# Kernel tuning notes

Hardware: AMD Instinct MI355X
Metric: run time of the kernel (lower is better)

Reference implementation:

```python
import jax, jax.numpy as jnp
import numpy as np

B, T, E, H = 1, 4096, 1024, 16
HD = E // H  # 64
SCALE = 8.0 / HD  # scaling='d' per Tensor Programs V


def setup_inputs() -> dict:
    key = jax.random.key(0)
    ks = jax.random.split(key, 7)
    s = 1.0 / np.sqrt(E)
    return {
        "q": jax.random.normal(ks[0], (B, T, E), jnp.float32),
        "k": jax.random.normal(ks[1], (B, T, E), jnp.float32),
        "v": jax.random.normal(ks[2], (B, T, E), jnp.float32),
        "Wq": jax.random.normal(ks[3], (E, E), jnp.float32) * s,
        "Wk": jax.random.normal(ks[4], (E, E), jnp.float32) * s,
        "Wv": jax.random.normal(ks[5], (E, E), jnp.float32) * s,
        "Wo": jax.random.normal(ks[6], (E, E), jnp.float32) * s,
    }


def reference(q, k, v, Wq, Wk, Wv, Wo):
    # bias-free linear projections (nn.Linear: y = x @ W.T)
    qp = q @ Wq.T
    kp = k @ Wk.T
    vp = v @ Wv.T
    # b t (h d) -> b h t d
    qh = qp.reshape(B, T, H, HD).transpose(0, 2, 1, 3)
    kh = kp.reshape(B, T, H, HD).transpose(0, 2, 1, 3)
    vh = vp.reshape(B, T, H, HD).transpose(0, 2, 1, 3)
    scores = jnp.einsum('bhqd,bhkd->bhqk', qh, kh) * SCALE
    # causal mask: positions k > q masked with -inf
    causal = jnp.tril(jnp.ones((T, T), dtype=bool))
    scores = jnp.where(causal[None, None], scores, -jnp.inf)
    probs = jax.nn.softmax(scores, axis=-1)
    out = jnp.einsum('bhqk,bhkd->bhqd', probs, vh)
    # b h t d -> b t (h d)
    out = out.transpose(0, 2, 1, 3).reshape(B, T, E)
    return out @ Wo.T
```

## Files before the change

kernel.cpp:

```cpp
#include <hip/hip_runtime.h>
#include <hip/hip_bf16.h>

#define T_DIM 4096
#define E_DIM 1024
#define H_DIM 16
#define HD_DIM 64
#define LOG2E_F 1.4426950408889634f
#define QSCALE_F (0.125f * LOG2E_F)

typedef __bf16 bf16_t;
typedef __bf16 bf16x8 __attribute__((ext_vector_type(8)));
typedef __bf16 bf16x4 __attribute__((ext_vector_type(4)));
typedef float  f32x4  __attribute__((ext_vector_type(4)));

__device__ inline void stage8(bf16_t* dst, const float* src) {
  const f32x4* s4 = (const f32x4*)src;
  f32x4 a = s4[0], b = s4[1];
  bf16x8 o;
  o[0] = (bf16_t)a[0]; o[1] = (bf16_t)a[1]; o[2] = (bf16_t)a[2]; o[3] = (bf16_t)a[3];
  o[4] = (bf16_t)b[0]; o[5] = (bf16_t)b[1]; o[6] = (bf16_t)b[2]; o[7] = (bf16_t)b[3];
  *(bf16x8*)dst = o;
}
__device__ inline void stage8(bf16_t* dst, const bf16_t* src) {
  *(bf16x8*)dst = *(const bf16x8*)src;
}

__device__ inline void gld_lds16(const bf16_t* g, bf16_t* l) {
  __builtin_amdgcn_global_load_lds(
      (const __attribute__((address_space(1))) unsigned int*)g,
      (__attribute__((address_space(3))) unsigned int*)l, 16, 0, 0);
}

__device__ inline float fexp2(float x) {
  float r;
  asm("v_exp_f32 %0, %1" : "=v"(r) : "v"(x));
  return r;
}

__device__ inline void block_sync() {
  asm volatile("" ::: "memory");
  __builtin_amdgcn_s_barrier();
  asm volatile("" ::: "memory");
}

__global__ __launch_bounds__(256) void cvt_all(
    const float* __restrict__ q, const float* __restrict__ k, const float* __restrict__ v,
    const float* __restrict__ Wq, const float* __restrict__ Wk,
    const float* __restrict__ Wv, const float* __restrict__ Wo,
    bf16_t* qb, bf16_t* kb, bf16_t* vb,
    bf16_t* Wqb, bf16_t* Wkb, bf16_t* Wvb, bf16_t* Wob) {
  for (int u = blockIdx.x * 256 + threadIdx.x; u < 2097152; u += gridDim.x * 256) {
    const float* s; bf16_t* d; int i;
    if (u < 1572864) {
      int seg = u >> 19, off = u & 524287;
      s = seg == 0 ? q : (seg == 1 ? k : v);
      d = seg == 0 ? qb : (seg == 1 ? kb : vb);
      i = off;
    } else {
      int w = u - 1572864;
      int seg = w >> 17, off = w & 131071;
      s = seg == 0 ? Wq : seg == 1 ? Wk : seg == 2 ? Wv : Wo;
      d = seg == 0 ? Wqb : seg == 1 ? Wkb : seg == 2 ? Wvb : Wob;
      i = off;
    }
    stage8(d + (size_t)i * 8, s + (size_t)i * 8);
  }
}

template <int MF, int NF, typename TC>
__device__ __forceinline__ void gemm_body(const bf16_t* __restrict__ A,
                                          const bf16_t* __restrict__ B,
                                          TC* __restrict__ C,
                                          int ldC, int bm, int bn, float cs) {
  constexpr int BM = 32 * MF, BN = 32 * NF;
  __shared__ alignas(16) bf16_t As[BM][64];
  __shared__ alignas(16) bf16_t Bs[BN][64];
  const int tid  = threadIdx.x;
  const int lane = tid & 63, w = tid >> 6;
  const int g = lane >> 4, l15 = lane & 15;
  const int wr = w >> 1, wc = w & 1;

  f32x4 acc[MF][NF] = {};

  for (int kt = 0; kt < 1024; kt += 64) {
    if (kt) __syncthreads();
#pragma unroll
    for (int p = 0; p < MF; ++p) {
      int s = p * 256 + tid;
      int row = s >> 3, c = s & 7;
      int cg = c ^ (row & 7);
      gld_lds16(&A[(size_t)(bm + row) * 1024 + kt + cg * 8], &As[0][0] + s * 8);
    }
#pragma unroll
    for (int p = 0; p < NF; ++p) {
      int s = p * 256 + tid;
      int row = s >> 3, c = s & 7;
      int cg = c ^ (row & 7);
      gld_lds16(&B[(size_t)(bn + row) * 1024 + kt + cg * 8], &Bs[0][0] + s * 8);
    }
    asm volatile("s_waitcnt vmcnt(0)" ::: "memory");
    __syncthreads();

#pragma unroll
    for (int hh = 0; hh < 2; ++hh) {
      bf16x8 af[MF], bfr[NF];
#pragma unroll
      for (int m = 0; m < MF; ++m) {
        int row = wr * (16 * MF) + m * 16 + l15;
        af[m] = *(const bf16x8*)(&As[0][0] + row * 64 + (((hh * 4 + g) ^ (row & 7)) * 8));
      }
#pragma unroll
      for (int n = 0; n < NF; ++n) {
        int row = wc * (16 * NF) + n * 16 + l15;
        bfr[n] = *(const bf16x8*)(&Bs[0][0] + row * 64 + (((hh * 4 + g) ^ (row & 7)) * 8));
      }
#pragma unroll
      for (int m = 0; m < MF; ++m)
#pragma unroll
        for (int n = 0; n < NF; ++n)
          acc[m][n] = __builtin_amdgcn_mfma_f32_16x16x32_bf16(af[m], bfr[n], acc[m][n], 0, 0, 0);
    }
  }

#pragma unroll
  for (int m = 0; m < MF; ++m)
#pragma unroll
    for (int n = 0; n < NF; ++n)
#pragma unroll
      for (int r = 0; r < 4; ++r) {
        int row = bm + wr * (16 * MF) + m * 16 + g * 4 + r;
        int col = bn + wc * (16 * NF) + n * 16 + l15;
        C[(size_t)row * ldC + col] = (TC)(acc[m][n][r] * cs);
      }
}

__global__ __launch_bounds__(256) void proj_qkv(
    const bf16_t* __restrict__ qb, const bf16_t* __restrict__ kb,
    const bf16_t* __restrict__ vb,
    const bf16_t* __restrict__ Wqb, const bf16_t* __restrict__ Wkb,
    const bf16_t* __restrict__ Wvb,
    bf16_t* Qp, bf16_t* Kp, bf16_t* Vt) {
  const int bid = blockIdx.x;
  const int which = bid >> 8, t = bid & 255;
  const bf16_t *A, *B; bf16_t* C; int ldC, bm, bn; float cs;
  if (which == 0) {
    A = qb;  B = Wqb; C = Qp; ldC = 1024;
    bm = (t >> 3) * 128; bn = (t & 7) * 128; cs = QSCALE_F;
  } else if (which == 1) {
    A = kb;  B = Wkb; C = Kp; ldC = 1024;
    bm = (t >> 3) * 128; bn = (t & 7) * 128; cs = 1.0f;
  } else {
    A = Wvb; B = vb;  C = Vt; ldC = 4096;
    bm = (t >> 5) * 128; bn = (t & 31) * 128; cs = 1.0f;
  }
  gemm_body<4, 4, bf16_t>(A, B, C, ldC, bm, bn, cs);
}

__global__ __launch_bounds__(256) void gemm_fin(const bf16_t* __restrict__ A,
                                                const bf16_t* __restrict__ B,
                                                float* __restrict__ C) {
  gemm_body<2, 4, float>(A, B, C, 1024, blockIdx.y * 64, blockIdx.x * 128, 1.0f);
}

template <typename TA, typename TB, typename TC>
__global__ __launch_bounds__(256) void gemm_bt(const TA* __restrict__ A,
                                               const TB* __restrict__ B,
                                               TC* __restrict__ C,
                                               int M, int N, int K, float cscale) {
  __shared__ alignas(16) bf16_t As[128][40];
  __shared__ alignas(16) bf16_t Bs[128][40];
  const int tid  = threadIdx.x;
  const int lane = tid & 63, w = tid >> 6;
  const int g = lane >> 4, l15 = lane & 15;
  const int wr = w >> 1, wc = w & 1;
  const int bm = blockIdx.y * 128, bn = blockIdx.x * 128;

  f32x4 acc[4][4] = {};

  for (int kt = 0; kt < K; kt += 32) {
    __syncthreads();
#pragma unroll
    for (int i = 0; i < 2; ++i) {
      int vv  = tid + i * 256;
      int row = vv >> 2, c8 = (vv & 3) * 8;
      stage8(&As[row][c8], &A[(size_t)(bm + row) * K + kt + c8]);
      stage8(&Bs[row][c8], &B[(size_t)(bn + row) * K + kt + c8]);
    }
    __syncthreads();

    bf16x8 af[4], bfr[4];
#pragma unroll
    for (int m = 0; m < 4; ++m)
      af[m] = *(const bf16x8*)&As[wr * 64 + m * 16 + l15][g * 8];
#pragma unroll
    for (int n = 0; n < 4; ++n)
      bfr[n] = *(const bf16x8*)&Bs[wc * 64 + n * 16 + l15][g * 8];
#pragma unroll
    for (int m = 0; m < 4; ++m)
#pragma unroll
      for (int n = 0; n < 4; ++n)
        acc[m][n] = __builtin_amdgcn_mfma_f32_16x16x32_bf16(af[m], bfr[n], acc[m][n], 0, 0, 0);
  }

#pragma unroll
  for (int m = 0; m < 4; ++m)
#pragma unroll
    for (int n = 0; n < 4; ++n)
#pragma unroll
      for (int r = 0; r < 4; ++r) {
        int row = bm + wr * 64 + m * 16 + g * 4 + r;
        int col = bn + wc * 64 + n * 16 + l15;
        C[(size_t)row * N + col] = (TC)(acc[m][n][r] * cscale);
      }
}

__global__ __launch_bounds__(256) void attn_fwd(const bf16_t* __restrict__ Qp,
                                                const bf16_t* __restrict__ Kp,
                                                const bf16_t* __restrict__ Vt,
                                                bf16_t* __restrict__ Oattn) {
  const int bid = blockIdx.x;
  const int h  = bid & 15;
  const int qi = 63 - (bid >> 4);
  const int tid = threadIdx.x, lane = tid & 63, w = tid >> 6;
  const int g = lane >> 4, l15 = lane & 15;
  const int qrow = qi * 64 + w * 16;

  __shared__ alignas(16) bf16_t Ks[2][64][64];
  __shared__ alignas(16) bf16_t Vs[3][64][64];
  __shared__ alignas(16) bf16_t Plds[4][16][72];

  bf16x8 qf[2];
  {
    const bf16_t* qp = &Qp[(size_t)(qrow + l15) * E_DIM + h * 64 + g * 8];
    qf[0] = *(const bf16x8*)qp;
    qf[1] = *(const bf16x8*)(qp + 32);
  }

  const int row0 = tid >> 3, c0 = tid & 7;
  const int cgo = (c0 ^ (row0 & 7)) * 8;
  const bf16_t* srcK0 = Kp + (size_t)row0 * E_DIM + h * 64 + cgo;
  const bf16_t* srcK1 = srcK0 + (size_t)32 * E_DIM;
  const bf16_t* srcV0 = Vt + (size_t)(h * 64 + row0) * T_DIM + cgo;
  const bf16_t* srcV1 = srcV0 + (size_t)32 * T_DIM;
  bf16_t* KsAll = &Ks[0][0][0];
  bf16_t* VsAll = &Vs[0][0][0];
  const size_t KADV = (size_t)64 * E_DIM;
  const int nt = qi + 1;

  auto issue = [&](int t) {
    bf16_t* kd = KsAll + (t & 1) * 4096;
    bf16_t* vd = VsAll + (t % 3) * 4096;
    gld_lds16(srcK0 + (size_t)t * KADV, kd + tid * 8);
    gld_lds16(srcK1 + (size_t)t * KADV, kd + (256 + tid) * 8);
    gld_lds16(srcV0 + (size_t)t * 64,   vd + tid * 8);
    gld_lds16(srcV1 + (size_t)t * 64,   vd + (256 + tid) * 8);
  };

  f32x4 acc[4] = {};
  float m_s = -1e30f, l_s = 0.f;

  auto pv = [&](int t) {
    const char* Vb = (const char*)(VsAll + (t % 3) * 4096);
    bf16x8 pf0 = *(const bf16x8*)&Plds[w][l15][g * 8];
    bf16x8 pf1 = *(const bf16x8*)&Plds[w][l15][32 + g * 8];
#pragma unroll
    for (int c = 0; c < 4; ++c) {
      const int vr = c * 16 + l15;
      const char* rp = Vb + vr * 128;
      const int sw = (vr & 7) << 4;
      bf16x8 v0 = *(const bf16x8*)(rp + ((g * 16) ^ sw));
      bf16x8 v1 = *(const bf16x8*)(rp + ((64 + g * 16) ^ sw));
      acc[c] = __builtin_amdgcn_mfma_f32_16x16x32_bf16(v0, pf0, acc[c], 0, 0, 0);
      acc[c] = __builtin_amdgcn_mfma_f32_16x16x32_bf16(v1, pf1, acc[c], 0, 0, 0);
    }
  };

  issue(0);

  for (int j = 0; j < nt; ++j) {
    asm volatile("s_waitcnt vmcnt(0)" ::: "memory");
    block_sync();
    if (j + 1 < nt) issue(j + 1);

    __builtin_amdgcn_s_setprio(1);
    if (j > 0) pv(j - 1);

    const char* Kb = (const char*)(KsAll + (j & 1) * 4096);
    f32x4 s[4] = {};
#pragma unroll
    for (int j16 = 0; j16 < 4; ++j16) {
      const int r0 = j16 * 16 + l15;
      const char* rp = Kb + r0 * 128;
      const int sw = (r0 & 7) << 4;
      bf16x8 k0 = *(const bf16x8*)(rp + ((g * 16) ^ sw));
      bf16x8 k1 = *(const bf16x8*)(rp + ((64 + g * 16) ^ sw));
      s[j16] = __builtin_amdgcn_mfma_f32_16x16x32_bf16(k0, qf[0], s[j16], 0, 0, 0);
      s[j16] = __builtin_amdgcn_mfma_f32_16x16x32_bf16(k1, qf[1], s[j16], 0, 0, 0);
    }
    __builtin_amdgcn_s_setprio(0);

    if (j == nt - 1) {
      const int kb = j * 64;
#pragma unroll
      for (int j16 = 0; j16 < 4; ++j16)
#pragma unroll
        for (int r = 0; r < 4; ++r)
          if (kb + j16 * 16 + g * 4 + r > qrow + l15) s[j16][r] = -1e30f;
    }

    float pmax = s[0][0];
#pragma unroll
    for (int j16 = 0; j16 < 4; ++j16)
#pragma unroll
      for (int r = 0; r < 4; ++r) pmax = fmaxf(pmax, s[j16][r]);
    pmax = fmaxf(pmax, __shfl_xor(pmax, 16));
    pmax = fmaxf(pmax, __shfl_xor(pmax, 32));

    if (!__all(pmax <= m_s + 11.0f)) {
      float mn = fmaxf(m_s, pmax);
      float sc = fexp2(m_s - mn);
      m_s = mn;
      l_s *= sc;
#pragma unroll
      for (int c = 0; c < 4; ++c)
#pragma unroll
        for (int r = 0; r < 4; ++r) acc[c][r] *= sc;
    }

    float ps = 0.f;
#pragma unroll
    for (int j16 = 0; j16 < 4; ++j16)
#pragma unroll
      for (int r = 0; r < 4; ++r) {
        s[j16][r] = fexp2(s[j16][r] - m_s);
        ps += s[j16][r];
      }
    ps += __shfl_xor(ps, 16);
    ps += __shfl_xor(ps, 32);
    l_s += ps;

#pragma unroll
    for (int j16 = 0; j16 < 4; ++j16) {
      bf16x4 pk;
      pk[0] = (bf16_t)s[j16][0]; pk[1] = (bf16_t)s[j16][1];
      pk[2] = (bf16_t)s[j16][2]; pk[3] = (bf16_t)s[j16][3];
      *(bf16x4*)&Plds[w][l15][j16 * 16 + g * 4] = pk;
    }
  }

  pv(nt - 1);

  const float inv = 1.0f / l_s;
#pragma unroll
  for (int c = 0; c < 4; ++c) {
    bf16x4 o;
#pragma unroll
    for (int r = 0; r < 4; ++r) o[r] = (bf16_t)(acc[c][r] * inv);
    *(bf16x4*)&Oattn[(size_t)(qrow + l15) * E_DIM + h * 64 + c * 16 + g * 4] = o;
  }
}

extern "C" void kernel_launch(void* const* d_in, const int* in_sizes, int n_in,
                              void* d_out, int out_size, void* d_ws, size_t ws_size,
                              hipStream_t stream) {
  const float* q  = (const float*)d_in[0];
  const float* k  = (const float*)d_in[1];
  const float* v  = (const float*)d_in[2];
  const float* Wq = (const float*)d_in[3];
  const float* Wk = (const float*)d_in[4];
  const float* Wv = (const float*)d_in[5];
  const float* Wo = (const float*)d_in[6];
  float* out = (float*)d_out;

  const size_t TE = (size_t)T_DIM * E_DIM;
  const size_t EE = (size_t)E_DIM * E_DIM;
  dim3 blk(256);

  if (ws_size >= (size_t)56 * 1024 * 1024) {
    bf16_t* qb  = (bf16_t*)d_ws;
    bf16_t* kb  = qb + TE;
    bf16_t* vb  = kb + TE;
    bf16_t* Wqb = vb + TE;
    bf16_t* Wkb = Wqb + EE;
    bf16_t* Wvb = Wkb + EE;
    bf16_t* Wob = Wvb + EE;
    bf16_t* Qp  = Wob + EE;
    bf16_t* Kp  = Qp + TE;
    bf16_t* Vt  = Kp + TE;
    bf16_t* Oa  = qb;

    cvt_all<<<2048, blk, 0, stream>>>(q, k, v, Wq, Wk, Wv, Wo,
                                      qb, kb, vb, Wqb, Wkb, Wvb, Wob);
    proj_qkv<<<dim3(768), blk, 0, stream>>>(qb, kb, vb, Wqb, Wkb, Wvb, Qp, Kp, Vt);
    attn_fwd<<<dim3(1024), blk, 0, stream>>>(Qp, Kp, Vt, Oa);
    gemm_fin<<<dim3(8, 64), blk, 0, stream>>>(Oa, Wob, out);
  } else {
    bf16_t* Qp = (bf16_t*)d_ws;
    bf16_t* Kp = Qp + TE;
    bf16_t* Vt = Kp + TE;
    bf16_t* Oa = Vt + TE;
    gemm_bt<float, float, bf16_t><<<dim3(8, 32), blk, 0, stream>>>(q, Wq, Qp, T_DIM, E_DIM, E_DIM, QSCALE_F);
    gemm_bt<float, float, bf16_t><<<dim3(8, 32), blk, 0, stream>>>(k, Wk, Kp, T_DIM, E_DIM, E_DIM, 1.0f);
    gemm_bt<float, float, bf16_t><<<dim3(32, 8), blk, 0, stream>>>(Wv, v, Vt, E_DIM, T_DIM, E_DIM, 1.0f);
    attn_fwd<<<dim3(1024), blk, 0, stream>>>(Qp, Kp, Vt, Oa);
    gemm_bt<bf16_t, float, float><<<dim3(8, 32), blk, 0, stream>>>(Oa, Wo, out, T_DIM, E_DIM, E_DIM, 1.0f);
  }
}
```

Before: 141.0 us.

## Halve attention KV tile to 32 keys and defer row-sum reduction

The attention kernel now steps through keys in 32-wide tiles instead of 64, so each iteration loads one K and one V chunk per thread, and the LDS buffers and the P buffer shrink with a new XOR swizzle. The per-lane partial row sum is kept local and reduced across lanes only once at the end, and the row-max shuffles run only when a rescale is needed. Masking is applied to every tile that overlaps the diagonal rather than only the last one. This lowers LDS use per block and per-iteration shuffle work, at the cost of twice as many iterations, each with a barrier and a wait on memory.

```diff
diff --git a/kernel.cpp b/kernel.cpp
--- a/kernel.cpp
+++ b/kernel.cpp
@@ -225,9 +225,9 @@
   const int g = lane >> 4, l15 = lane & 15;
   const int qrow = qi * 64 + w * 16;
 
-  __shared__ alignas(16) bf16_t Ks[2][64][64];
-  __shared__ alignas(16) bf16_t Vs[3][64][64];
-  __shared__ alignas(16) bf16_t Plds[4][16][72];
+  __shared__ alignas(16) bf16_t Ks[2][32][64];
+  __shared__ alignas(16) bf16_t Vs[3][64][32];
+  __shared__ alignas(16) bf16_t Plds[4][16][32];
 
   bf16x8 qf[2];
   {
@@ -236,42 +236,34 @@
     qf[1] = *(const bf16x8*)(qp + 32);
   }
 
-  const int row0 = tid >> 3, c0 = tid & 7;
-  const int cgo = (c0 ^ (row0 & 7)) * 8;
-  const bf16_t* srcK0 = Kp + (size_t)row0 * E_DIM + h * 64 + cgo;
-  const bf16_t* srcK1 = srcK0 + (size_t)32 * E_DIM;
-  const bf16_t* srcV0 = Vt + (size_t)(h * 64 + row0) * T_DIM + cgo;
-  const bf16_t* srcV1 = srcV0 + (size_t)32 * T_DIM;
+  const int krow = tid >> 3;
+  const int kcg  = ((tid & 7) ^ (krow & 7)) * 8;
+  const bf16_t* srcK = Kp + (size_t)krow * E_DIM + h * 64 + kcg;
+  const int vrow = tid >> 2;
+  const int vcg  = ((tid & 3) ^ (vrow & 3)) * 8;
+  const bf16_t* srcV = Vt + (size_t)(h * 64 + vrow) * T_DIM + vcg;
   bf16_t* KsAll = &Ks[0][0][0];
   bf16_t* VsAll = &Vs[0][0][0];
-  const size_t KADV = (size_t)64 * E_DIM;
-  const int nt = qi + 1;
+  const size_t KADV = (size_t)32 * E_DIM;
+  const int nt = 2 * qi + 2;
 
   auto issue = [&](int t) {
-    bf16_t* kd = KsAll + (t & 1) * 4096;
-    bf16_t* vd = VsAll + (t % 3) * 4096;
-    gld_lds16(srcK0 + (size_t)t * KADV, kd + tid * 8);
-    gld_lds16(srcK1 + (size_t)t * KADV, kd + (256 + tid) * 8);
-    gld_lds16(srcV0 + (size_t)t * 64,   vd + tid * 8);
-    gld_lds16(srcV1 + (size_t)t * 64,   vd + (256 + tid) * 8);
+    gld_lds16(srcK + (size_t)t * KADV, KsAll + (t & 1) * 2048 + tid * 8);
+    gld_lds16(srcV + (size_t)t * 32,   VsAll + (t % 3) * 2048 + tid * 8);
   };
 
   f32x4 acc[4] = {};
-  float m_s = -1e30f, l_s = 0.f;
-
+  float m_s = -1e30f, l_p = 0.f;
+
+  const int psw = (g ^ (l15 & 3)) << 4;
   auto pv = [&](int t) {
-    const char* Vb = (const char*)(VsAll + (t % 3) * 4096);
-    bf16x8 pf0 = *(const bf16x8*)&Plds[w][l15][g * 8];
-    bf16x8 pf1 = *(const bf16x8*)&Plds[w][l15][32 + g * 8];
+    const char* Vb = (const char*)(VsAll + (t % 3) * 2048);
+    bf16x8 pf0 = *(const bf16x8*)((const char*)&Plds[w][l15][0] + psw);
 #pragma unroll
     for (int c = 0; c < 4; ++c) {
       const int vr = c * 16 + l15;
-      const char* rp = Vb + vr * 128;
-      const int sw = (vr & 7) << 4;
-      bf16x8 v0 = *(const bf16x8*)(rp + ((g * 16) ^ sw));
-      bf16x8 v1 = *(const bf16x8*)(rp + ((64 + g * 16) ^ sw));
+      bf16x8 v0 = *(const bf16x8*)(Vb + vr * 64 + psw);
       acc[c] = __builtin_amdgcn_mfma_f32_16x16x32_bf16(v0, pf0, acc[c], 0, 0, 0);
-      acc[c] = __builtin_amdgcn_mfma_f32_16x16x32_bf16(v1, pf1, acc[c], 0, 0, 0);
     }
   };
 
@@ -285,10 +277,10 @@
     __builtin_amdgcn_s_setprio(1);
     if (j > 0) pv(j - 1);
 
-    const char* Kb = (const char*)(KsAll + (j & 1) * 4096);
-    f32x4 s[4] = {};
-#pragma unroll
-    for (int j16 = 0; j16 < 4; ++j16) {
+    const char* Kb = (const char*)(KsAll + (j & 1) * 2048);
+    f32x4 s[2] = {};
+#pragma unroll
+    for (int j16 = 0; j16 < 2; ++j16) {
       const int r0 = j16 * 16 + l15;
       const char* rp = Kb + r0 * 128;
       const int sw = (r0 & 7) << 4;
@@ -299,28 +291,24 @@
     }
     __builtin_amdgcn_s_setprio(0);
 
-    if (j == nt - 1) {
-      const int kb = j * 64;
-#pragma unroll
-      for (int j16 = 0; j16 < 4; ++j16)
+    const int kb = j * 32;
+    if (kb + 31 > qrow) {
+#pragma unroll
+      for (int j16 = 0; j16 < 2; ++j16)
 #pragma unroll
         for (int r = 0; r < 4; ++r)
           if (kb + j16 * 16 + g * 4 + r > qrow + l15) s[j16][r] = -1e30f;
     }
 
-    float pmax = s[0][0];
-#pragma unroll
-    for (int j16 = 0; j16 < 4; ++j16)
-#pragma unroll
-      for (int r = 0; r < 4; ++r) pmax = fmaxf(pmax, s[j16][r]);
-    pmax = fmaxf(pmax, __shfl_xor(pmax, 16));
-    pmax = fmaxf(pmax, __shfl_xor(pmax, 32));
-
+    float pmax = fmaxf(fmaxf(fmaxf(s[0][0], s[0][1]), fmaxf(s[0][2], s[0][3])),
+                       fmaxf(fmaxf(s[1][0], s[1][1]), fmaxf(s[1][2], s[1][3])));
     if (!__all(pmax <= m_s + 11.0f)) {
-      float mn = fmaxf(m_s, pmax);
+      float rm = fmaxf(pmax, __shfl_xor(pmax, 16));
+      rm = fmaxf(rm, __shfl_xor(rm, 32));
+      float mn = fmaxf(m_s, rm);
       float sc = fexp2(m_s - mn);
       m_s = mn;
-      l_s *= sc;
+      l_p *= sc;
 #pragma unroll
       for (int c = 0; c < 4; ++c)
 #pragma unroll
@@ -329,28 +317,29 @@
 
     float ps = 0.f;
 #pragma unroll
-    for (int j16 = 0; j16 < 4; ++j16)
+    for (int j16 = 0; j16 < 2; ++j16)
 #pragma unroll
       for (int r = 0; r < 4; ++r) {
         s[j16][r] = fexp2(s[j16][r] - m_s);
         ps += s[j16][r];
       }
-    ps += __shfl_xor(ps, 16);
-    ps += __shfl_xor(ps, 32);
-    l_s += ps;
-
-#pragma unroll
-    for (int j16 = 0; j16 < 4; ++j16) {
+    l_p += ps;
+
+#pragma unroll
+    for (int j16 = 0; j16 < 2; ++j16) {
       bf16x4 pk;
       pk[0] = (bf16_t)s[j16][0]; pk[1] = (bf16_t)s[j16][1];
       pk[2] = (bf16_t)s[j16][2]; pk[3] = (bf16_t)s[j16][3];
-      *(bf16x4*)&Plds[w][l15][j16 * 16 + g * 4] = pk;
+      *(bf16x4*)&Plds[w][l15][(((2 * j16 + (g >> 1)) ^ (l15 & 3)) * 8) + (g & 1) * 4] = pk;
     }
   }
 
   pv(nt - 1);
 
-  const float inv = 1.0f / l_s;
+  float lt = l_p;
+  lt += __shfl_xor(lt, 16);
+  lt += __shfl_xor(lt, 32);
+  const float inv = 1.0f / lt;
 #pragma unroll
   for (int c = 0; c < 4; ++c) {
     bf16x4 o;
```

New measurement: 151.4 us. +7.4%, slower.

## Pair causal query tiles per block for balanced attention work

Applied to the files above, without the earlier changes.

Each attention block now handles two query tiles, one at 63-ii and one at ii, so every block does the same total number of key tiles (65). The grid is halved to 512 blocks. This removes the load imbalance and tail effect of causal attention, at the cost of fewer blocks and a serial second pass with an extra barrier. The row max cross-lane shuffle now runs only inside the rescale branch. The row-sum reduction is moved out of the loop to the end of each pass.

```diff
diff --git a/kernel.cpp b/kernel.cpp
--- a/kernel.cpp
+++ b/kernel.cpp
@@ -220,21 +220,13 @@
                                                 bf16_t* __restrict__ Oattn) {
   const int bid = blockIdx.x;
   const int h  = bid & 15;
-  const int qi = 63 - (bid >> 4);
+  const int ii = bid >> 4;
   const int tid = threadIdx.x, lane = tid & 63, w = tid >> 6;
   const int g = lane >> 4, l15 = lane & 15;
-  const int qrow = qi * 64 + w * 16;
 
   __shared__ alignas(16) bf16_t Ks[2][64][64];
   __shared__ alignas(16) bf16_t Vs[3][64][64];
   __shared__ alignas(16) bf16_t Plds[4][16][72];
-
-  bf16x8 qf[2];
-  {
-    const bf16_t* qp = &Qp[(size_t)(qrow + l15) * E_DIM + h * 64 + g * 8];
-    qf[0] = *(const bf16x8*)qp;
-    qf[1] = *(const bf16x8*)(qp + 32);
-  }
 
   const int row0 = tid >> 3, c0 = tid & 7;
   const int cgo = (c0 ^ (row0 & 7)) * 8;
@@ -245,7 +237,6 @@
   bf16_t* KsAll = &Ks[0][0][0];
   bf16_t* VsAll = &Vs[0][0][0];
   const size_t KADV = (size_t)64 * E_DIM;
-  const int nt = qi + 1;
 
   auto issue = [&](int t) {
     bf16_t* kd = KsAll + (t & 1) * 4096;
@@ -256,8 +247,8 @@
     gld_lds16(srcV1 + (size_t)t * 64,   vd + (256 + tid) * 8);
   };
 
-  f32x4 acc[4] = {};
-  float m_s = -1e30f, l_s = 0.f;
+  f32x4 acc[4];
+  float m_s, l_p;
 
   auto pv = [&](int t) {
     const char* Vb = (const char*)(VsAll + (t % 3) * 4096);
@@ -275,88 +266,108 @@
     }
   };
 
-  issue(0);
-
-  for (int j = 0; j < nt; ++j) {
-    asm volatile("s_waitcnt vmcnt(0)" ::: "memory");
-    block_sync();
-    if (j + 1 < nt) issue(j + 1);
-
-    __builtin_amdgcn_s_setprio(1);
-    if (j > 0) pv(j - 1);
-
-    const char* Kb = (const char*)(KsAll + (j & 1) * 4096);
-    f32x4 s[4] = {};
-#pragma unroll
-    for (int j16 = 0; j16 < 4; ++j16) {
-      const int r0 = j16 * 16 + l15;
-      const char* rp = Kb + r0 * 128;
-      const int sw = (r0 & 7) << 4;
-      bf16x8 k0 = *(const bf16x8*)(rp + ((g * 16) ^ sw));
-      bf16x8 k1 = *(const bf16x8*)(rp + ((64 + g * 16) ^ sw));
-      s[j16] = __builtin_amdgcn_mfma_f32_16x16x32_bf16(k0, qf[0], s[j16], 0, 0, 0);
-      s[j16] = __builtin_amdgcn_mfma_f32_16x16x32_bf16(k1, qf[1], s[j16], 0, 0, 0);
-    }
-    __builtin_amdgcn_s_setprio(0);
-
-    if (j == nt - 1) {
-      const int kb = j * 64;
+  for (int pass = 0; pass < 2; ++pass) {
+    const int qi = pass ? ii : 63 - ii;
+    const int qrow = qi * 64 + w * 16;
+    const int nt = qi + 1;
+
+    bf16x8 qf[2];
+    {
+      const bf16_t* qp = &Qp[(size_t)(qrow + l15) * E_DIM + h * 64 + g * 8];
+      qf[0] = *(const bf16x8*)qp;
+      qf[1] = *(const bf16x8*)(qp + 32);
+    }
+#pragma unroll
+    for (int c = 0; c < 4; ++c)
+#pragma unroll
+      for (int r = 0; r < 4; ++r) acc[c][r] = 0.f;
+    m_s = -1e30f; l_p = 0.f;
+
+    if (pass) block_sync();
+    issue(0);
+
+    for (int j = 0; j < nt; ++j) {
+      asm volatile("s_waitcnt vmcnt(0)" ::: "memory");
+      block_sync();
+      if (j + 1 < nt) issue(j + 1);
+
+      __builtin_amdgcn_s_setprio(1);
+      if (j > 0) pv(j - 1);
+
+      const char* Kb = (const char*)(KsAll + (j & 1) * 4096);
+      f32x4 s[4] = {};
+#pragma unroll
+      for (int j16 = 0; j16 < 4; ++j16) {
+        const int r0 = j16 * 16 + l15;
+        const char* rp = Kb + r0 * 128;
+        const int sw = (r0 & 7) << 4;
+        bf16x8 k0 = *(const bf16x8*)(rp + ((g * 16) ^ sw));
+        bf16x8 k1 = *(const bf16x8*)(rp + ((64 + g * 16) ^ sw));
+        s[j16] = __builtin_amdgcn_mfma_f32_16x16x32_bf16(k0, qf[0], s[j16], 0, 0, 0);
+        s[j16] = __builtin_amdgcn_mfma_f32_16x16x32_bf16(k1, qf[1], s[j16], 0, 0, 0);
+      }
+      __builtin_amdgcn_s_setprio(0);
+
+      if (j == nt - 1) {
+        const int kb = j * 64;
+#pragma unroll
+        for (int j16 = 0; j16 < 4; ++j16)
+#pragma unroll
+          for (int r = 0; r < 4; ++r)
+            if (kb + j16 * 16 + g * 4 + r > qrow + l15) s[j16][r] = -1e30f;
+      }
+
+      float pmax = s[0][0];
 #pragma unroll
       for (int j16 = 0; j16 < 4; ++j16)
 #pragma unroll
-        for (int r = 0; r < 4; ++r)
-          if (kb + j16 * 16 + g * 4 + r > qrow + l15) s[j16][r] = -1e30f;
-    }
-
-    float pmax = s[0][0];
-#pragma unroll
-    for (int j16 = 0; j16 < 4; ++j16)
-#pragma unroll
-      for (int r = 0; r < 4; ++r) pmax = fmaxf(pmax, s[j16][r]);
-    pmax = fmaxf(pmax, __shfl_xor(pmax, 16));
-    pmax = fmaxf(pmax, __shfl_xor(pmax, 32));
-
-    if (!__all(pmax <= m_s + 11.0f)) {
-      float mn = fmaxf(m_s, pmax);
-      float sc = fexp2(m_s - mn);
-      m_s = mn;
-      l_s *= sc;
-#pragma unroll
-      for (int c = 0; c < 4; ++c)
-#pragma unroll
-        for (int r = 0; r < 4; ++r) acc[c][r] *= sc;
-    }
-
-    float ps = 0.f;
-#pragma unroll
-    for (int j16 = 0; j16 < 4; ++j16)
-#pragma unroll
-      for (int r = 0; r < 4; ++r) {
-        s[j16][r] = fexp2(s[j16][r] - m_s);
-        ps += s[j16][r];
-      }
-    ps += __shfl_xor(ps, 16);
-    ps += __shfl_xor(ps, 32);
-    l_s += ps;
-
-#pragma unroll
-    for (int j16 = 0; j16 < 4; ++j16) {
-      bf16x4 pk;
-      pk[0] = (bf16_t)s[j16][0]; pk[1] = (bf16_t)s[j16][1];
-      pk[2] = (bf16_t)s[j16][2]; pk[3] = (bf16_t)s[j16][3];
-      *(bf16x4*)&Plds[w][l15][j16 * 16 + g * 4] = pk;
-    }
-  }
-
-  pv(nt - 1);
-
-  const float inv = 1.0f / l_s;
-#pragma unroll
-  for (int c = 0; c < 4; ++c) {
-    bf16x4 o;
-#pragma unroll
-    for (int r = 0; r < 4; ++r) o[r] = (bf16_t)(acc[c][r] * inv);
-    *(bf16x4*)&Oattn[(size_t)(qrow + l15) * E_DIM + h * 64 + c * 16 + g * 4] = o;
+        for (int r = 0; r < 4; ++r) pmax = fmaxf(pmax, s[j16][r]);
+
+      if (!__all(pmax <= m_s + 11.0f)) {
+        float rm = fmaxf(pmax, __shfl_xor(pmax, 16));
+        rm = fmaxf(rm, __shfl_xor(rm, 32));
+        float mn = fmaxf(m_s, rm);
+        float sc = fexp2(m_s - mn);
+        m_s = mn;
+        l_p *= sc;
+#pragma unroll
+        for (int c = 0; c < 4; ++c)
+#pragma unroll
+          for (int r = 0; r < 4; ++r) acc[c][r] *= sc;
+      }
+
+      float ps = 0.f;
+#pragma unroll
+      for (int j16 = 0; j16 < 4; ++j16)
+#pragma unroll
+        for (int r = 0; r < 4; ++r) {
+          s[j16][r] = fexp2(s[j16][r] - m_s);
+          ps += s[j16][r];
+        }
+      l_p += ps;
+
+#pragma unroll
+      for (int j16 = 0; j16 < 4; ++j16) {
+        bf16x4 pk;
+        pk[0] = (bf16_t)s[j16][0]; pk[1] = (bf16_t)s[j16][1];
+        pk[2] = (bf16_t)s[j16][2]; pk[3] = (bf16_t)s[j16][3];
+        *(bf16x4*)&Plds[w][l15][j16 * 16 + g * 4] = pk;
+      }
+    }
+
+    pv(nt - 1);
+
+    float lt = l_p;
+    lt += __shfl_xor(lt, 16);
+    lt += __shfl_xor(lt, 32);
+    const float inv = 1.0f / lt;
+#pragma unroll
+    for (int c = 0; c < 4; ++c) {
+      bf16x4 o;
+#pragma unroll
+      for (int r = 0; r < 4; ++r) o[r] = (bf16_t)(acc[c][r] * inv);
+      *(bf16x4*)&Oattn[(size_t)(qrow + l15) * E_DIM + h * 64 + c * 16 + g * 4] = o;
+    }
   }
 }
 
@@ -392,7 +403,7 @@
     cvt_all<<<2048, blk, 0, stream>>>(q, k, v, Wq, Wk, Wv, Wo,
                                       qb, kb, vb, Wqb, Wkb, Wvb, Wob);
     proj_qkv<<<dim3(768), blk, 0, stream>>>(qb, kb, vb, Wqb, Wkb, Wvb, Qp, Kp, Vt);
-    attn_fwd<<<dim3(1024), blk, 0, stream>>>(Qp, Kp, Vt, Oa);
+    attn_fwd<<<dim3(512), blk, 0, stream>>>(Qp, Kp, Vt, Oa);
     gemm_fin<<<dim3(8, 64), blk, 0, stream>>>(Oa, Wob, out);
   } else {
     bf16_t* Qp = (bf16_t*)d_ws;
@@ -402,7 +413,7 @@
     gemm_bt<float, float, bf16_t><<<dim3(8, 32), blk, 0, stream>>>(q, Wq, Qp, T_DIM, E_DIM, E_DIM, QSCALE_F);
     gemm_bt<float, float, bf16_t><<<dim3(8, 32), blk, 0, stream>>>(k, Wk, Kp, T_DIM, E_DIM, E_DIM, 1.0f);
     gemm_bt<float, float, bf16_t><<<dim3(32, 8), blk, 0, stream>>>(Wv, v, Vt, E_DIM, T_DIM, E_DIM, 1.0f);
-    attn_fwd<<<dim3(1024), blk, 0, stream>>>(Qp, Kp, Vt, Oa);
+    attn_fwd<<<dim3(512), blk, 0, stream>>>(Qp, Kp, Vt, Oa);
     gemm_bt<bf16_t, float, float><<<dim3(8, 32), blk, 0, stream>>>(Oa, Wo, out, T_DIM, E_DIM, E_DIM, 1.0f);
   }
 }
```

Result: faster. 131.6 us (-6.7%).

## Use 32x32 MFMA attention tiles with 128-row query blocks and MFMA row sums

Applied to the files above, without the earlier changes.

Rewrites the attention kernel so each block handles 128 query rows, with 32 rows per wave, and uses 32x32x16 MFMAs in place of 16x16x32. This halves the grid and doubles K/V tile reuse per block load. The softmax row sum now comes from an extra MFMA against a ones vector instead of shuffle reductions. The causal schedule is remapped to pair heavy and light query blocks, and the P LDS layout is swizzled. In exchange it uses more accumulator registers and adds an extra MFMA per PV step, and the larger blocks may reduce occupancy and load balance.

```diff
diff --git a/kernel.cpp b/kernel.cpp
--- a/kernel.cpp
+++ b/kernel.cpp
@@ -12,6 +12,7 @@
 typedef __bf16 bf16x8 __attribute__((ext_vector_type(8)));
 typedef __bf16 bf16x4 __attribute__((ext_vector_type(4)));
 typedef float  f32x4  __attribute__((ext_vector_type(4)));
+typedef float  f32x16 __attribute__((ext_vector_type(16)));
 
 __device__ inline void stage8(bf16_t* dst, const float* src) {
   const f32x4* s4 = (const f32x4*)src;
@@ -219,22 +220,27 @@
                                                 const bf16_t* __restrict__ Vt,
                                                 bf16_t* __restrict__ Oattn) {
   const int bid = blockIdx.x;
-  const int h  = bid & 15;
-  const int qi = 63 - (bid >> 4);
+  const int h   = bid & 15;
+  const int idx = bid >> 4;
+  const int qi  = idx < 16 ? 31 - idx : idx - 16;
   const int tid = threadIdx.x, lane = tid & 63, w = tid >> 6;
-  const int g = lane >> 4, l15 = lane & 15;
-  const int qrow = qi * 64 + w * 16;
+  const int ql = lane & 31, hl = lane >> 5;
+  const int qrow = qi * 128 + w * 32;
 
   __shared__ alignas(16) bf16_t Ks[2][64][64];
   __shared__ alignas(16) bf16_t Vs[3][64][64];
-  __shared__ alignas(16) bf16_t Plds[4][16][72];
-
-  bf16x8 qf[2];
+  __shared__ alignas(16) bf16_t Plds[4][32][64];
+
+  bf16x8 qf[4];
   {
-    const bf16_t* qp = &Qp[(size_t)(qrow + l15) * E_DIM + h * 64 + g * 8];
-    qf[0] = *(const bf16x8*)qp;
-    qf[1] = *(const bf16x8*)(qp + 32);
-  }
+    const bf16_t* qp = &Qp[(size_t)(qrow + ql) * E_DIM + h * 64 + 8 * hl];
+#pragma unroll
+    for (int ds = 0; ds < 4; ++ds) qf[ds] = *(const bf16x8*)(qp + ds * 16);
+  }
+
+  bf16x8 ones;
+#pragma unroll
+  for (int i = 0; i < 8; ++i) ones[i] = (bf16_t)1.0f;
 
   const int row0 = tid >> 3, c0 = tid & 7;
   const int cgo = (c0 ^ (row0 & 7)) * 8;
@@ -245,7 +251,7 @@
   bf16_t* KsAll = &Ks[0][0][0];
   bf16_t* VsAll = &Vs[0][0][0];
   const size_t KADV = (size_t)64 * E_DIM;
-  const int nt = qi + 1;
+  const int nt = 2 * qi + 2;
 
   auto issue = [&](int t) {
     bf16_t* kd = KsAll + (t & 1) * 4096;
@@ -256,22 +262,26 @@
     gld_lds16(srcV1 + (size_t)t * 64,   vd + (256 + tid) * 8);
   };
 
-  f32x4 acc[4] = {};
-  float m_s = -1e30f, l_s = 0.f;
+  f32x16 acc0 = {}, acc1 = {};
+  f32x16 acc_l = {};
+  float m_s = -1e30f;
+
+  const char* Pw = (const char*)&Plds[w][0][0];
+  const int x7 = ql & 7;
 
   auto pv = [&](int t) {
     const char* Vb = (const char*)(VsAll + (t % 3) * 4096);
-    bf16x8 pf0 = *(const bf16x8*)&Plds[w][l15][g * 8];
-    bf16x8 pf1 = *(const bf16x8*)&Plds[w][l15][32 + g * 8];
-#pragma unroll
-    for (int c = 0; c < 4; ++c) {
-      const int vr = c * 16 + l15;
-      const char* rp = Vb + vr * 128;
-      const int sw = (vr & 7) << 4;
-      bf16x8 v0 = *(const bf16x8*)(rp + ((g * 16) ^ sw));
-      bf16x8 v1 = *(const bf16x8*)(rp + ((64 + g * 16) ^ sw));
-      acc[c] = __builtin_amdgcn_mfma_f32_16x16x32_bf16(v0, pf0, acc[c], 0, 0, 0);
-      acc[c] = __builtin_amdgcn_mfma_f32_16x16x32_bf16(v1, pf1, acc[c], 0, 0, 0);
+    bf16x8 pf[4];
+#pragma unroll
+    for (int ks = 0; ks < 4; ++ks)
+      pf[ks] = *(const bf16x8*)(Pw + ql * 128 + (((2 * ks + hl) ^ x7) << 4));
+#pragma unroll
+    for (int ks = 0; ks < 4; ++ks) {
+      bf16x8 v0 = *(const bf16x8*)(Vb + ql * 128        + (((2 * ks + hl) ^ x7) << 4));
+      bf16x8 v1 = *(const bf16x8*)(Vb + (32 + ql) * 128 + (((2 * ks + hl) ^ x7) << 4));
+      acc0 = __builtin_amdgcn_mfma_f32_32x32x16_bf16(v0, pf[ks], acc0, 0, 0, 0);
+      acc1 = __builtin_amdgcn_mfma_f32_32x32x16_bf16(v1, pf[ks], acc1, 0, 0, 0);
+      acc_l = __builtin_amdgcn_mfma_f32_32x32x16_bf16(ones, pf[ks], acc_l, 0, 0, 0);
     }
   };
 
@@ -286,77 +296,84 @@
     if (j > 0) pv(j - 1);
 
     const char* Kb = (const char*)(KsAll + (j & 1) * 4096);
-    f32x4 s[4] = {};
-#pragma unroll
-    for (int j16 = 0; j16 < 4; ++j16) {
-      const int r0 = j16 * 16 + l15;
-      const char* rp = Kb + r0 * 128;
-      const int sw = (r0 & 7) << 4;
-      bf16x8 k0 = *(const bf16x8*)(rp + ((g * 16) ^ sw));
-      bf16x8 k1 = *(const bf16x8*)(rp + ((64 + g * 16) ^ sw));
-      s[j16] = __builtin_amdgcn_mfma_f32_16x16x32_bf16(k0, qf[0], s[j16], 0, 0, 0);
-      s[j16] = __builtin_amdgcn_mfma_f32_16x16x32_bf16(k1, qf[1], s[j16], 0, 0, 0);
+    f32x16 s0 = {}, s1 = {};
+#pragma unroll
+    for (int ds = 0; ds < 4; ++ds) {
+      bf16x8 k0 = *(const bf16x8*)(Kb + ql * 128        + (((2 * ds + hl) ^ x7) << 4));
+      bf16x8 k1 = *(const bf16x8*)(Kb + (32 + ql) * 128 + (((2 * ds + hl) ^ x7) << 4));
+      s0 = __builtin_amdgcn_mfma_f32_32x32x16_bf16(k0, qf[ds], s0, 0, 0, 0);
+      s1 = __builtin_amdgcn_mfma_f32_32x32x16_bf16(k1, qf[ds], s1, 0, 0, 0);
     }
     __builtin_amdgcn_s_setprio(0);
 
-    if (j == nt - 1) {
-      const int kb = j * 64;
-#pragma unroll
-      for (int j16 = 0; j16 < 4; ++j16)
-#pragma unroll
-        for (int r = 0; r < 4; ++r)
-          if (kb + j16 * 16 + g * 4 + r > qrow + l15) s[j16][r] = -1e30f;
-    }
-
-    float pmax = s[0][0];
-#pragma unroll
-    for (int j16 = 0; j16 < 4; ++j16)
-#pragma unroll
-      for (int r = 0; r < 4; ++r) pmax = fmaxf(pmax, s[j16][r]);
-    pmax = fmaxf(pmax, __shfl_xor(pmax, 16));
-    pmax = fmaxf(pmax, __shfl_xor(pmax, 32));
+    const int kb = j * 64;
+    if (kb + 63 > qrow) {
+#pragma unroll
+      for (int i = 0; i < 16; ++i) {
+        int krow = kb + (i & 3) + 8 * (i >> 2) + 4 * hl;
+        if (krow > qrow + ql)      s0[i] = -1e30f;
+        if (krow + 32 > qrow + ql) s1[i] = -1e30f;
+      }
+    }
+
+    float pmax;
+    {
+      float t0 = fmaxf(fmaxf(s0[0], s0[1]),  fmaxf(s0[2], s0[3]));
+      float t1 = fmaxf(fmaxf(s0[4], s0[5]),  fmaxf(s0[6], s0[7]));
+      float t2 = fmaxf(fmaxf(s0[8], s0[9]),  fmaxf(s0[10], s0[11]));
+      float t3 = fmaxf(fmaxf(s0[12], s0[13]), fmaxf(s0[14], s0[15]));
+      float t4 = fmaxf(fmaxf(s1[0], s1[1]),  fmaxf(s1[2], s1[3]));
+      float t5 = fmaxf(fmaxf(s1[4], s1[5]),  fmaxf(s1[6], s1[7]));
+      float t6 = fmaxf(fmaxf(s1[8], s1[9]),  fmaxf(s1[10], s1[11]));
+      float t7 = fmaxf(fmaxf(s1[12], s1[13]), fmaxf(s1[14], s1[15]));
+      pmax = fmaxf(fmaxf(fmaxf(t0, t1), fmaxf(t2, t3)),
+                   fmaxf(fmaxf(t4, t5), fmaxf(t6, t7)));
+    }
 
     if (!__all(pmax <= m_s + 11.0f)) {
-      float mn = fmaxf(m_s, pmax);
+      float rm = fmaxf(pmax, __shfl_xor(pmax, 32));
+      float mn = fmaxf(m_s, rm);
       float sc = fexp2(m_s - mn);
       m_s = mn;
-      l_s *= sc;
-#pragma unroll
-      for (int c = 0; c < 4; ++c)
-#pragma unroll
-        for (int r = 0; r < 4; ++r) acc[c][r] *= sc;
-    }
-
-    float ps = 0.f;
-#pragma unroll
-    for (int j16 = 0; j16 < 4; ++j16)
+#pragma unroll
+      for (int i = 0; i < 16; ++i) {
+        acc0[i] *= sc; acc1[i] *= sc; acc_l[i] *= sc;
+      }
+    }
+
+#pragma unroll
+    for (int i = 0; i < 16; ++i) {
+      s0[i] = fexp2(s0[i] - m_s);
+      s1[i] = fexp2(s1[i] - m_s);
+    }
+
+#pragma unroll
+    for (int rq = 0; rq < 4; ++rq) {
+      bf16x4 p0, p1;
 #pragma unroll
       for (int r = 0; r < 4; ++r) {
-        s[j16][r] = fexp2(s[j16][r] - m_s);
-        ps += s[j16][r];
-      }
-    ps += __shfl_xor(ps, 16);
-    ps += __shfl_xor(ps, 32);
-    l_s += ps;
-
-#pragma unroll
-    for (int j16 = 0; j16 < 4; ++j16) {
-      bf16x4 pk;
-      pk[0] = (bf16_t)s[j16][0]; pk[1] = (bf16_t)s[j16][1];
-      pk[2] = (bf16_t)s[j16][2]; pk[3] = (bf16_t)s[j16][3];
-      *(bf16x4*)&Plds[w][l15][j16 * 16 + g * 4] = pk;
+        p0[r] = (bf16_t)s0[rq * 4 + r];
+        p1[r] = (bf16_t)s1[rq * 4 + r];
+      }
+      *(bf16x4*)((char*)Pw + ql * 128 + ((rq ^ x7) << 4)       + 8 * hl) = p0;
+      *(bf16x4*)((char*)Pw + ql * 128 + (((4 + rq) ^ x7) << 4) + 8 * hl) = p1;
     }
   }
 
   pv(nt - 1);
 
-  const float inv = 1.0f / l_s;
-#pragma unroll
-  for (int c = 0; c < 4; ++c) {
-    bf16x4 o;
-#pragma unroll
-    for (int r = 0; r < 4; ++r) o[r] = (bf16_t)(acc[c][r] * inv);
-    *(bf16x4*)&Oattn[(size_t)(qrow + l15) * E_DIM + h * 64 + c * 16 + g * 4] = o;
+  const float inv = 1.0f / acc_l[0];
+#pragma unroll
+  for (int rq = 0; rq < 4; ++rq) {
+    bf16x4 o0, o1;
+#pragma unroll
+    for (int r = 0; r < 4; ++r) {
+      o0[r] = (bf16_t)(acc0[rq * 4 + r] * inv);
+      o1[r] = (bf16_t)(acc1[rq * 4 + r] * inv);
+    }
+    bf16_t* orow = &Oattn[(size_t)(qrow + ql) * E_DIM + h * 64];
+    *(bf16x4*)(orow + 8 * rq + 4 * hl)      = o0;
+    *(bf16x4*)(orow + 32 + 8 * rq + 4 * hl) = o1;
   }
 }
 
@@ -392,7 +409,7 @@
     cvt_all<<<2048, blk, 0, stream>>>(q, k, v, Wq, Wk, Wv, Wo,
                                       qb, kb, vb, Wqb, Wkb, Wvb, Wob);
     proj_qkv<<<dim3(768), blk, 0, stream>>>(qb, kb, vb, Wqb, Wkb, Wvb, Qp, Kp, Vt);
-    attn_fwd<<<dim3(1024), blk, 0, stream>>>(Qp, Kp, Vt, Oa);
+    attn_fwd<<<dim3(512), blk, 0, stream>>>(Qp, Kp, Vt, Oa);
     gemm_fin<<<dim3(8, 64), blk, 0, stream>>>(Oa, Wob, out);
   } else {
     bf16_t* Qp = (bf16_t*)d_ws;
@@ -402,7 +419,7 @@
     gemm_bt<float, float, bf16_t><<<dim3(8, 32), blk, 0, stream>>>(q, Wq, Qp, T_DIM, E_DIM, E_DIM, QSCALE_F);
     gemm_bt<float, float, bf16_t><<<dim3(8, 32), blk, 0, stream>>>(k, Wk, Kp, T_DIM, E_DIM, E_DIM, 1.0f);
     gemm_bt<float, float, bf16_t><<<dim3(32, 8), blk, 0, stream>>>(Wv, v, Vt, E_DIM, T_DIM, E_DIM, 1.0f);
-    attn_fwd<<<dim3(1024), blk, 0, stream>>>(Qp, Kp, Vt, Oa);
+    attn_fwd<<<dim3(512), blk, 0, stream>>>(Qp, Kp, Vt, Oa);
     gemm_bt<bf16_t, float, float><<<dim3(8, 32), blk, 0, stream>>>(Oa, Wo, out, T_DIM, E_DIM, E_DIM, 1.0f);
   }
 }
```

Result: slower. 169.1 us (+20.0%).
